# Kernel tuning notes

Hardware: AMD Instinct MI355X
Metric: run time of the kernel (lower is better)

## Reference

```python
import jax, jax.numpy as jnp
import numpy as np


def log_g(x):
    # log of g(x) = x+0.5 for x>=0, sigmoid(x) for x<0, computed stably
    return jnp.where(x >= 0, jnp.log(jax.nn.relu(x) + 0.5), -jax.nn.softplus(-x))


def setup_inputs() -> dict:
    key = jax.random.key(0)
    k1, k2 = jax.random.split(key)
    B, S, D = 4, 4096, 1024
    x = jax.random.normal(k1, (B, S, D), dtype=jnp.float32)
    W = jax.random.normal(k2, (D, 3 * D), dtype=jnp.float32) * (1.0 / np.sqrt(D))
    return {"x": x, "W": W}


def reference(x, W):
    # fused gate projection: [B,S,D] @ [D,3D] -> f_gate, i_gate, hidden
    gates = jnp.einsum('bsd,de->bse', x, W)
    f_gate, i_gate, hidden = jnp.split(gates, 3, axis=-1)

    # log-space normalized gates: log_f = log(sig(f)/(sig(f)+sig(i))) etc.
    diff = jax.nn.softplus(-f_gate) - jax.nn.softplus(-i_gate)
    log_f = -jax.nn.softplus(diff)
    log_i = -jax.nn.softplus(-diff)
    log_tilde_h = log_g(hidden)

    log_values = log_i + log_tilde_h
    # parallel scan in log space over seq axis (axis=1)
    a_star = jnp.cumsum(log_f, axis=1)
    log_h0_plus_b_star = jax.lax.cumlogsumexp(log_values - a_star, axis=1)
    h = jnp.exp(a_star + log_h0_plus_b_star)  # [B,S,D]
    return h  # to_out is Identity for expansion_factor == 1.0
```

## Files before the change

kernel.cpp:

```cpp
#include <hip/hip_runtime.h>
#include <hip/hip_fp16.h>
#include <cstdint>

typedef _Float16 half8  __attribute__((ext_vector_type(8)));
typedef _Float16 half4v __attribute__((ext_vector_type(4)));
typedef _Float16 half2v __attribute__((ext_vector_type(2)));
typedef float    floatx4 __attribute__((ext_vector_type(4)));

constexpr int Bb = 4, Ss = 4096, Dd = 1024;
constexpr int Mdim = Bb * Ss;
constexpr int Ndim = 3 * Dd;
constexpr int Kdim = Dd;
constexpr int CH = 128, LCH = Ss / CH;

__device__ __forceinline__ void gload_lds16(const void* g, void* l) {
  __builtin_amdgcn_global_load_lds(
      (const __attribute__((address_space(1))) uint32_t*)g,
      (__attribute__((address_space(3))) uint32_t*)l, 16, 0, 0);
}

__device__ __forceinline__ void gate_fv(float fg, float ig, float hg,
                                        float& fw, float& v) {
  float ef = __expf(fminf(-fg, 40.f));
  float ei = __expf(fminf(-ig, 40.f));
  float r  = __builtin_amdgcn_rcpf(2.f + ef + ei);
  fw = (1.f + ei) * r;
  float iw = (1.f + ef) * r;
  float g  = hg >= 0.f ? hg + 0.5f
                       : __builtin_amdgcn_rcpf(1.f + __expf(fminf(-hg, 40.f)));
  v = iw * g;
}

__global__ __launch_bounds__(256) void cvt_x_k(const float* __restrict__ X,
                                               _Float16* __restrict__ X16, int n4) {
  for (int i = blockIdx.x * blockDim.x + threadIdx.x; i < n4;
       i += gridDim.x * blockDim.x) {
    float4 v = ((const float4*)X)[i];
    half4v o = {(_Float16)v.x, (_Float16)v.y, (_Float16)v.z, (_Float16)v.w};
    ((half4v*)X16)[i] = o;
  }
}

__global__ __launch_bounds__(256) void cvt_wT_k(const float* __restrict__ W,
                                                _Float16* __restrict__ WT) {
  __shared__ float tile[32][33];
  int tx = threadIdx.x & 31, ty = threadIdx.x >> 5;
  int n0 = blockIdx.x * 32, k0 = blockIdx.y * 32;
#pragma unroll
  for (int j = 0; j < 4; ++j) {
    int k = ty + j * 8;
    tile[k][tx] = W[(int64_t)(k0 + k) * Ndim + n0 + tx];
  }
  __syncthreads();
#pragma unroll
  for (int j = 0; j < 4; ++j) {
    int nl = ty + j * 8;
    WT[(int64_t)(n0 + nl) * Kdim + k0 + tx] = (_Float16)tile[tx][nl];
  }
}

constexpr int GBM = 256, GBN = 256, GBK = 64;
constexpr int NT = Kdim / GBK;

__global__ __launch_bounds__(512, 2) void gemm8_k(const _Float16* __restrict__ A,
                                                  const _Float16* __restrict__ BT,
                                                  _Float16* __restrict__ Cg) {
  extern __shared__ char lds[];
  const int tid = threadIdx.x;
  const int wid = tid >> 6, lane = tid & 63;
  const int wm = wid >> 2, wn = wid & 3;
  const int l15 = lane & 15, lq = lane >> 4;

  int wg = blockIdx.x;
  wg = (wg & 7) * 96 + (wg >> 3);
  const int n0 = (wg % 12) * GBN;
  const int m0 = (wg / 12) * GBM;

  int aO[4], bO[2];
#pragma unroll
  for (int mi = 0; mi < 4; ++mi) {
    int r = wm * 64 + mi * 16 + l15;
    aO[mi] = r * 128 + ((lq ^ (r & 7)) << 4);
  }
#pragma unroll
  for (int ni = 0; ni < 2; ++ni) {
    int r = wn * 32 + ni * 16 + l15;
    bO[ni] = r * 128 + ((lq ^ (r & 7)) << 4);
  }

  const int srr = (wid << 3) + (lane >> 3);
  const int ss = lane & 7;
  const _Float16* Abase = A + (size_t)m0 * Kdim;
  const _Float16* Bbase = BT + (size_t)n0 * Kdim;

  auto stage = [&](const _Float16* gsrc, int ldsHalfBase) {
#pragma unroll
    for (int round = 0; round < 2; ++round) {
      int r = (round << 6) + srr;
      int c = ss ^ (r & 7);
      gload_lds16(gsrc + (size_t)r * Kdim + (c << 3),
                  lds + ldsHalfBase + (round << 13) + (wid << 10));
    }
  };

  floatx4 acc[8][4] = {};

  stage(Abase, 0);
  stage(Bbase, 32768);
  stage(Bbase + 128 * Kdim, 49152);
  stage(Abase + 128 * Kdim, 16384);
  stage(Abase + 64, 65536);
  stage(Bbase + 64, 65536 + 32768);
  asm volatile("s_waitcnt vmcnt(4)" ::: "memory");
  __builtin_amdgcn_s_barrier();

  for (int kt = 0; kt < NT; ++kt) {
    const int cur = (kt & 1) << 16, nxt = ((kt + 1) & 1) << 16;
    const _Float16* Akt1 = Abase + (kt + 1) * GBK;
    const _Float16* Bkt1 = Bbase + (kt + 1) * GBK;
    const _Float16* Akt2 = Abase + (kt + 2) * GBK;
    const _Float16* Bkt2 = Bbase + (kt + 2) * GBK;

    half8 a[4][2], b0[2][2], b1[2][2];

#pragma unroll
    for (int mi = 0; mi < 4; ++mi)
#pragma unroll
      for (int ks = 0; ks < 2; ++ks)
        a[mi][ks] = *(const half8*)(lds + cur + (aO[mi] ^ (ks << 6)));
#pragma unroll
    for (int ni = 0; ni < 2; ++ni)
#pragma unroll
      for (int ks = 0; ks < 2; ++ks) {
        b0[ni][ks] = *(const half8*)(lds + cur + 32768 + (bO[ni] ^ (ks << 6)));
        b1[ni][ks] = *(const half8*)(lds + cur + 49152 + (bO[ni] ^ (ks << 6)));
      }
    if (kt + 1 < NT) stage(Bkt1 + 128 * Kdim, nxt + 49152);

    __builtin_amdgcn_s_setprio(1);
#pragma unroll
    for (int ks = 0; ks < 2; ++ks)
#pragma unroll
      for (int mi = 0; mi < 4; ++mi)
#pragma unroll
        for (int ni = 0; ni < 2; ++ni)
          acc[mi][ni] = __builtin_amdgcn_mfma_f32_16x16x32_f16(
              a[mi][ks], b0[ni][ks], acc[mi][ni], 0, 0, 0);
    __builtin_amdgcn_s_setprio(0);
    if (kt + 1 < NT) stage(Akt1 + 128 * Kdim, nxt + 16384);

    __builtin_amdgcn_s_setprio(1);
#pragma unroll
    for (int ks = 0; ks < 2; ++ks)
#pragma unroll
      for (int mi = 0; mi < 4; ++mi)
#pragma unroll
        for (int ni = 0; ni < 2; ++ni)
          acc[mi][2 + ni] = __builtin_amdgcn_mfma_f32_16x16x32_f16(
              a[mi][ks], b1[ni][ks], acc[mi][2 + ni], 0, 0, 0);
    __builtin_amdgcn_s_setprio(0);

    __builtin_amdgcn_s_barrier();

#pragma unroll
    for (int mi = 0; mi < 4; ++mi)
#pragma unroll
      for (int ks = 0; ks < 2; ++ks)
        a[mi][ks] = *(const half8*)(lds + cur + 16384 + (aO[mi] ^ (ks << 6)));
    if (kt + 2 < NT) stage(Akt2, cur + 0);

    __builtin_amdgcn_s_setprio(1);
#pragma unroll
    for (int ks = 0; ks < 2; ++ks)
#pragma unroll
      for (int mi = 0; mi < 4; ++mi)
#pragma unroll
        for (int ni = 0; ni < 2; ++ni)
          acc[4 + mi][ni] = __builtin_amdgcn_mfma_f32_16x16x32_f16(
              a[mi][ks], b0[ni][ks], acc[4 + mi][ni], 0, 0, 0);
    __builtin_amdgcn_s_setprio(0);
    if (kt + 2 < NT) stage(Bkt2, cur + 32768);

    __builtin_amdgcn_s_setprio(1);
#pragma unroll
    for (int ks = 0; ks < 2; ++ks)
#pragma unroll
      for (int mi = 0; mi < 4; ++mi)
#pragma unroll
        for (int ni = 0; ni < 2; ++ni)
          acc[4 + mi][2 + ni] = __builtin_amdgcn_mfma_f32_16x16x32_f16(
              a[mi][ks], b1[ni][ks], acc[4 + mi][2 + ni], 0, 0, 0);
    __builtin_amdgcn_s_setprio(0);

    if (kt < NT - 2) {
      asm volatile("s_waitcnt vmcnt(4)" ::: "memory");
      __builtin_amdgcn_s_barrier();
    } else if (kt == NT - 2) {
      asm volatile("s_waitcnt vmcnt(0)" ::: "memory");
      __builtin_amdgcn_s_barrier();
    }
  }

#pragma unroll
  for (int mf = 0; mf < 8; ++mf) {
    int row = m0 + ((mf >> 2) << 7) + wm * 64 + ((mf & 3) << 4) + (lq << 2);
#pragma unroll
    for (int nf = 0; nf < 4; ++nf) {
      int col = n0 + ((nf >> 1) << 7) + wn * 32 + ((nf & 1) << 4) + l15;
#pragma unroll
      for (int r = 0; r < 4; ++r)
        Cg[(size_t)(row + r) * Ndim + col] = (_Float16)acc[mf][nf][r];
    }
  }
}

__global__ __launch_bounds__(256) void scan1_k(const _Float16* __restrict__ G,
                                               float* __restrict__ Fc,
                                               float* __restrict__ Hc) {
  int d = threadIdx.x * 4;
  int c = blockIdx.y, b = blockIdx.z;
  const _Float16* g = G + (int64_t)(b * Ss + c * LCH) * Ndim + d;
  float h[4] = {0.f, 0.f, 0.f, 0.f};
  float F[4] = {1.f, 1.f, 1.f, 1.f};
#pragma unroll 4
  for (int s = 0; s < LCH; ++s) {
    half4v fg = *(const half4v*)(g);
    half4v ig = *(const half4v*)(g + Dd);
    half4v hg = *(const half4v*)(g + 2 * Dd);
#pragma unroll
    for (int j = 0; j < 4; ++j) {
      float fw, v;
      gate_fv((float)fg[j], (float)ig[j], (float)hg[j], fw, v);
      h[j] = fmaf(fw, h[j], v);
      F[j] *= fw;
    }
    g += Ndim;
  }
  int co = (b * CH + c) * Dd + d;
  *(floatx4*)(Fc + co) = *(floatx4*)F;
  *(floatx4*)(Hc + co) = *(floatx4*)h;
}

__global__ __launch_bounds__(256) void scan2_k(const float* __restrict__ Fc,
                                               const float* __restrict__ Hc,
                                               float* __restrict__ Carry) {
  int idx = blockIdx.x * 256 + threadIdx.x;
  int b = idx >> 10, d = idx & (Dd - 1);
  float carry = 0.f;
#pragma unroll 8
  for (int c = 0; c < CH; ++c) {
    int co = (b * CH + c) * Dd + d;
    Carry[co] = carry;
    carry = fmaf(Fc[co], carry, Hc[co]);
  }
}

__global__ __launch_bounds__(256) void scan3_k(const _Float16* __restrict__ G,
                                               const float* __restrict__ Carry,
                                               float* __restrict__ Out) {
  int d = threadIdx.x * 4;
  int c = blockIdx.y, b = blockIdx.z;
  int64_t row0 = (int64_t)(b * Ss + c * LCH);
  const _Float16* g = G + row0 * Ndim + d;
  float* o = Out + row0 * Dd + d;
  int co = (b * CH + c) * Dd + d;
  floatx4 hv = *(const floatx4*)(Carry + co);
  float h[4] = {hv[0], hv[1], hv[2], hv[3]};
#pragma unroll 4
  for (int s = 0; s < LCH; ++s) {
    half4v fg = *(const half4v*)(g);
    half4v ig = *(const half4v*)(g + Dd);
    half4v hg = *(const half4v*)(g + 2 * Dd);
#pragma unroll
    for (int j = 0; j < 4; ++j) {
      float fw, v;
      gate_fv((float)fg[j], (float)ig[j], (float)hg[j], fw, v);
      h[j] = fmaf(fw, h[j], v);
    }
    *(floatx4*)o = *(floatx4*)h;
    g += Ndim;
    o += Dd;
  }
}

extern "C" void kernel_launch(void* const* d_in, const int* in_sizes, int n_in,
                              void* d_out, int out_size, void* d_ws, size_t ws_size,
                              hipStream_t stream) {
  const float* x = (const float*)d_in[0];
  const float* W = (const float*)d_in[1];
  float* out = (float*)d_out;

  char* ws = (char*)d_ws;
  size_t off = 0;
  auto alloc = [&](size_t bytes) {
    char* p = ws + off;
    off += (bytes + 255) & ~size_t(255);
    return p;
  };
  _Float16* x16    = (_Float16*)alloc((size_t)Mdim * Kdim * 2);
  _Float16* w16t   = (_Float16*)alloc((size_t)Ndim * Kdim * 2);
  _Float16* gates  = (_Float16*)alloc((size_t)Mdim * Ndim * 2);
  float* Fc        = (float*)alloc((size_t)Bb * CH * Dd * 4);
  float* Hc        = (float*)alloc((size_t)Bb * CH * Dd * 4);
  float* Carry     = (float*)alloc((size_t)Bb * CH * Dd * 4);
  if (off > ws_size) return;

  cvt_x_k<<<2048, 256, 0, stream>>>(x, x16, Mdim * Kdim / 4);
  cvt_wT_k<<<dim3(Ndim / 32, Kdim / 32), 256, 0, stream>>>(W, w16t);
  gemm8_k<<<dim3((Mdim / GBM) * (Ndim / GBN)), 512, 131072, stream>>>(x16, w16t, gates);
  scan1_k<<<dim3(1, CH, Bb), 256, 0, stream>>>(gates, Fc, Hc);
  scan2_k<<<(Bb * Dd) / 256, 256, 0, stream>>>(Fc, Hc, Carry);
  scan3_k<<<dim3(1, CH, Bb), 256, 0, stream>>>(gates, Carry, out);
}
```

Baseline: 193.3 us.

## Cache fp16 forget/value pairs in scan pass 1 and double chunk count

The first scan pass now writes the computed forget weight and value as an interleaved fp16 pair per element into a buffer that aliases the no-longer-needed x16/w16t conversion buffers. The third pass reads only these 4 bytes per element instead of re-reading 6 bytes of gates and recomputing the exponentials. Pass 1 also rounds fw and v to fp16 before accumulating, so both passes use identical values. The chunk count is raised from 128 to 256 for more parallelism in the scan kernels. The cost is an extra write stream in pass 1, fp16 rounding of the gate weights, and a longer sequential carry pass.

```diff
diff --git a/kernel.cpp b/kernel.cpp
--- a/kernel.cpp
+++ b/kernel.cpp
@@ -4,14 +4,13 @@
 
 typedef _Float16 half8  __attribute__((ext_vector_type(8)));
 typedef _Float16 half4v __attribute__((ext_vector_type(4)));
-typedef _Float16 half2v __attribute__((ext_vector_type(2)));
 typedef float    floatx4 __attribute__((ext_vector_type(4)));
 
 constexpr int Bb = 4, Ss = 4096, Dd = 1024;
 constexpr int Mdim = Bb * Ss;
 constexpr int Ndim = 3 * Dd;
 constexpr int Kdim = Dd;
-constexpr int CH = 128, LCH = Ss / CH;
+constexpr int CH = 256, LCH = Ss / CH;
 
 __device__ __forceinline__ void gload_lds16(const void* g, void* l) {
   __builtin_amdgcn_global_load_lds(
@@ -215,11 +214,14 @@
 }
 
 __global__ __launch_bounds__(256) void scan1_k(const _Float16* __restrict__ G,
+                                               _Float16* __restrict__ fv,
                                                float* __restrict__ Fc,
                                                float* __restrict__ Hc) {
   int d = threadIdx.x * 4;
   int c = blockIdx.y, b = blockIdx.z;
-  const _Float16* g = G + (int64_t)(b * Ss + c * LCH) * Ndim + d;
+  int64_t m0 = (int64_t)(b * Ss + c * LCH);
+  const _Float16* g = G + m0 * Ndim + d;
+  _Float16* fvp = fv + (m0 * Dd + d) * 2;
   float h[4] = {0.f, 0.f, 0.f, 0.f};
   float F[4] = {1.f, 1.f, 1.f, 1.f};
 #pragma unroll 4
@@ -227,14 +229,21 @@
     half4v fg = *(const half4v*)(g);
     half4v ig = *(const half4v*)(g + Dd);
     half4v hg = *(const half4v*)(g + 2 * Dd);
+    half8 o;
 #pragma unroll
     for (int j = 0; j < 4; ++j) {
       float fw, v;
       gate_fv((float)fg[j], (float)ig[j], (float)hg[j], fw, v);
-      h[j] = fmaf(fw, h[j], v);
-      F[j] *= fw;
+      _Float16 fh = (_Float16)fw, vh = (_Float16)v;
+      o[2 * j] = fh;
+      o[2 * j + 1] = vh;
+      float fr = (float)fh, vr = (float)vh;
+      h[j] = fmaf(fr, h[j], vr);
+      F[j] *= fr;
     }
+    *(half8*)fvp = o;
     g += Ndim;
+    fvp += Dd * 2;
   }
   int co = (b * CH + c) * Dd + d;
   *(floatx4*)(Fc + co) = *(floatx4*)F;
@@ -255,30 +264,25 @@
   }
 }
 
-__global__ __launch_bounds__(256) void scan3_k(const _Float16* __restrict__ G,
+__global__ __launch_bounds__(256) void scan3_k(const _Float16* __restrict__ fv,
                                                const float* __restrict__ Carry,
                                                float* __restrict__ Out) {
   int d = threadIdx.x * 4;
   int c = blockIdx.y, b = blockIdx.z;
-  int64_t row0 = (int64_t)(b * Ss + c * LCH);
-  const _Float16* g = G + row0 * Ndim + d;
-  float* o = Out + row0 * Dd + d;
+  int64_t m0 = (int64_t)(b * Ss + c * LCH);
+  const _Float16* fvp = fv + (m0 * Dd + d) * 2;
+  float* o = Out + m0 * Dd + d;
   int co = (b * CH + c) * Dd + d;
   floatx4 hv = *(const floatx4*)(Carry + co);
   float h[4] = {hv[0], hv[1], hv[2], hv[3]};
 #pragma unroll 4
   for (int s = 0; s < LCH; ++s) {
-    half4v fg = *(const half4v*)(g);
-    half4v ig = *(const half4v*)(g + Dd);
-    half4v hg = *(const half4v*)(g + 2 * Dd);
-#pragma unroll
-    for (int j = 0; j < 4; ++j) {
-      float fw, v;
-      gate_fv((float)fg[j], (float)ig[j], (float)hg[j], fw, v);
-      h[j] = fmaf(fw, h[j], v);
-    }
+    half8 p = *(const half8*)fvp;
+#pragma unroll
+    for (int j = 0; j < 4; ++j)
+      h[j] = fmaf((float)p[2 * j], h[j], (float)p[2 * j + 1]);
     *(floatx4*)o = *(floatx4*)h;
-    g += Ndim;
+    fvp += Dd * 2;
     o += Dd;
   }
 }
@@ -297,18 +301,20 @@
     off += (bytes + 255) & ~size_t(255);
     return p;
   };
-  _Float16* x16    = (_Float16*)alloc((size_t)Mdim * Kdim * 2);
-  _Float16* w16t   = (_Float16*)alloc((size_t)Ndim * Kdim * 2);
   _Float16* gates  = (_Float16*)alloc((size_t)Mdim * Ndim * 2);
   float* Fc        = (float*)alloc((size_t)Bb * CH * Dd * 4);
   float* Hc        = (float*)alloc((size_t)Bb * CH * Dd * 4);
   float* Carry     = (float*)alloc((size_t)Bb * CH * Dd * 4);
+  char* uni        = alloc((size_t)Mdim * Dd * 2 * 2);
+  _Float16* x16    = (_Float16*)uni;
+  _Float16* w16t   = (_Float16*)(uni + (size_t)Mdim * Kdim * 2);
+  _Float16* fv     = (_Float16*)uni;
   if (off > ws_size) return;
 
   cvt_x_k<<<2048, 256, 0, stream>>>(x, x16, Mdim * Kdim / 4);
   cvt_wT_k<<<dim3(Ndim / 32, Kdim / 32), 256, 0, stream>>>(W, w16t);
   gemm8_k<<<dim3((Mdim / GBM) * (Ndim / GBN)), 512, 131072, stream>>>(x16, w16t, gates);
-  scan1_k<<<dim3(1, CH, Bb), 256, 0, stream>>>(gates, Fc, Hc);
+  scan1_k<<<dim3(1, CH, Bb), 256, 0, stream>>>(gates, fv, Fc, Hc);
   scan2_k<<<(Bb * Dd) / 256, 256, 0, stream>>>(Fc, Hc, Carry);
-  scan3_k<<<dim3(1, CH, Bb), 256, 0, stream>>>(gates, Carry, out);
-}
+  scan3_k<<<dim3(1, CH, Bb), 256, 0, stream>>>(fv, Carry, out);
+}
```

After: 197.1 us. 2.0% more time.
